# Kernel optimization log

Hardware: AMD Instinct MI355X
Metric: run time of the kernel (lower is better)

## Reference

```python
import jax, jax.numpy as jnp
import numpy as np

B, S, HID = 2, 2048, 2048
NH, NKV, D = 16, 4, 128  # heads, kv heads, dim_per_head
ROPE_BASE = 10000.0


def setup_inputs() -> dict:
    key = jax.random.key(0)
    ks = jax.random.split(key, 5)
    x = jax.random.normal(ks[0], (B, S, HID), jnp.float32)
    wq = jax.random.normal(ks[1], (HID, NH * D), jnp.float32) * 0.02
    wk = jax.random.normal(ks[2], (HID, NKV * D), jnp.float32) * 0.02
    wv = jax.random.normal(ks[3], (HID, NKV * D), jnp.float32) * 0.02
    wo = jax.random.normal(ks[4], (NH * D, HID), jnp.float32) * 0.02
    inv_freq = 1.0 / (ROPE_BASE ** (jnp.arange(0, D, 2, dtype=jnp.float32) / D))
    freqs = jnp.outer(jnp.arange(S, dtype=jnp.float32), inv_freq)  # [S, D/2]
    cos, sin = jnp.cos(freqs), jnp.sin(freqs)
    mask = jnp.tril(jnp.ones((S, S), dtype=bool))  # causal, True = attend
    return {"x": x, "wq": wq, "wk": wk, "wv": wv, "wo": wo,
            "cos": cos, "sin": sin, "mask": mask}


def _rope_interleave(t, cos, sin):
    # t: [B, H, S, D]; cos/sin: [S, D/2]; interleaved pairs (even, odd)
    te, to = t[..., ::2], t[..., 1::2]
    c, s = cos[None, None], sin[None, None]
    re = te * c - to * s
    ro = to * c + te * s
    return jnp.stack([re, ro], axis=-1).reshape(t.shape)


def reference(x, wq, wk, wv, wo, cos, sin, mask):
    b, s, _ = x.shape
    # QKV projections + shape(): [B, S, hid] -> [B, H, S, D]
    q = (x @ wq).reshape(b, s, NH, D).transpose(0, 2, 1, 3)
    k = (x @ wk).reshape(b, s, NKV, D).transpose(0, 2, 1, 3)
    v = (x @ wv).reshape(b, s, NKV, D).transpose(0, 2, 1, 3)
    q = _rope_interleave(q, cos, sin)
    k = _rope_interleave(k, cos, sin)
    # GQA: repeat each kv head heads//heads_kv times consecutively
    rep = NH // NKV
    k = jnp.repeat(k, rep, axis=1)
    v = jnp.repeat(v, rep, axis=1)
    scores = jnp.einsum('bhqd,bhkd->bhqk', q, k) * (D ** -0.5)
    scores = scores.astype(jnp.float32)
    scores = jnp.where(mask[None, None], scores, jnp.finfo(jnp.float32).min)
    attn = jax.nn.softmax(scores, axis=-1).astype(x.dtype)
    ctx = jnp.einsum('bhqk,bhkd->bhqd', attn, v)
    ctx = ctx.transpose(0, 2, 1, 3).reshape(b, s, NH * D)  # unshape()
    return ctx @ wo
```

## Files before the change

kernel.cpp:

```cpp
#include <hip/hip_runtime.h>
#include <hip/hip_bf16.h>
#include <math.h>

#define S_LEN 2048
#define HIDW 2048
#define NHEAD 16
#define NKVH 4
#define HD 128
#define NB 2
#define MROWS (NB * S_LEN)
#define QKVN (NHEAD * HD + 2 * NKVH * HD)
#define KOFF (NHEAD * HD)
#define VOFF (NHEAD * HD + NKVH * HD)

typedef __bf16 bf16_t;
typedef __bf16 bf16x8_t __attribute__((ext_vector_type(8)));
typedef float f32x4_t __attribute__((ext_vector_type(4)));

__device__ __forceinline__ void gload_lds16(const bf16_t* g, bf16_t* l) {
  __builtin_amdgcn_global_load_lds(
      (const __attribute__((address_space(1))) void*)g,
      (__attribute__((address_space(3))) void*)l, 16, 0, 0);
}

__device__ __forceinline__ f32x4_t zero4() {
  f32x4_t z = {0.f, 0.f, 0.f, 0.f};
  return z;
}

__device__ __forceinline__ float fexp2(float x) {
#if __has_builtin(__builtin_amdgcn_exp2f)
  return __builtin_amdgcn_exp2f(x);
#else
  return exp2f(x);
#endif
}

__global__ __launch_bounds__(256) void k_cvt8(const float* __restrict__ in,
                                              bf16_t* __restrict__ out, int n8) {
  int i = blockIdx.x * 256 + threadIdx.x;
  if (i >= n8) return;
  const float4* p = (const float4*)(in + (size_t)i * 8);
  float4 a = p[0], b = p[1];
  bf16x8_t r;
  r[0] = (bf16_t)a.x; r[1] = (bf16_t)a.y; r[2] = (bf16_t)a.z; r[3] = (bf16_t)a.w;
  r[4] = (bf16_t)b.x; r[5] = (bf16_t)b.y; r[6] = (bf16_t)b.z; r[7] = (bf16_t)b.w;
  *(bf16x8_t*)(out + (size_t)i * 8) = r;
}

__global__ __launch_bounds__(256) void k_tr_cvt(const float* __restrict__ in,
                                                bf16_t* __restrict__ out, int R, int C) {
  __shared__ float t[32][33];
  int c0 = blockIdx.x * 32, r0 = blockIdx.y * 32;
  int tx = threadIdx.x & 31, ty = threadIdx.x >> 5;
#pragma unroll
  for (int rr = ty; rr < 32; rr += 8) t[rr][tx] = in[(size_t)(r0 + rr) * C + c0 + tx];
  __syncthreads();
#pragma unroll
  for (int rr = ty; rr < 32; rr += 8)
    out[(size_t)(c0 + rr) * R + r0 + tx] = (bf16_t)t[tx][rr];
}

__global__ __launch_bounds__(512, 2) void k_gemm_qkv8(const bf16_t* __restrict__ A,
                                                      const bf16_t* __restrict__ Bt,
                                                      bf16_t* __restrict__ qkv,
                                                      const float* __restrict__ cosT,
                                                      const float* __restrict__ sinT) {
  __shared__ bf16_t As[2][16384];
  __shared__ bf16_t Bs[2][16384];
  const int K = HIDW, N = QKVN;
  int tid = threadIdx.x;
  int lane = tid & 63, wid = tid >> 6;
  int l15 = lane & 15, lg = lane >> 4;
  int wrb = (wid >> 2) * 128;
  int wcb = (wid & 3) * 64;
  int ah = wid >> 2;
  int bh2 = wcb >> 7;
  int brow0 = wcb & 64;

  int qx = gridDim.x >> 3;
  int lin = blockIdx.x;
  int wg = (lin & 7) * qx + (lin >> 3);
  int row0 = (wg / 12) * 256, col0 = (wg % 12) * 256;

  int srow = tid >> 3;
  int scol = ((tid & 7) ^ (srow & 7)) * 8;
  const bf16_t* Ag = A + (size_t)(row0 + srow) * K + scol;
  const bf16_t* Bg = Bt + (size_t)(col0 + srow) * K + scol;

  f32x4_t acc[8][4];
#pragma unroll
  for (int i = 0; i < 8; i++)
#pragma unroll
    for (int j = 0; j < 4; j++) acc[i][j] = zero4();

  int xr = (l15 & 7) << 4;
  const int nk = K >> 6;

  auto stA = [&](int tt, int h, int u) {
    gload_lds16(Ag + (size_t)(h * 128 + u * 64) * K + (size_t)tt * 64,
                As[tt & 1] + h * 8192 + u * 4096 + tid * 8);
  };
  auto stB = [&](int tt, int h, int u) {
    gload_lds16(Bg + (size_t)(h * 128 + u * 64) * K + (size_t)tt * 64,
                Bs[tt & 1] + h * 8192 + u * 4096 + tid * 8);
  };

  stB(0, 0, 0); stB(0, 0, 1); stA(0, 0, 0); stA(0, 0, 1);
  stB(0, 1, 0); stB(0, 1, 1); stA(0, 1, 0); stA(0, 1, 1);
  stB(1, 0, 0); stB(1, 0, 1); stA(1, 0, 0); stA(1, 0, 1);
  stB(1, 1, 0); stB(1, 1, 1);
  asm volatile("s_waitcnt vmcnt(10)" ::: "memory");
  __builtin_amdgcn_s_barrier();
  __builtin_amdgcn_sched_barrier(0);

  for (int t = 0; t < nk; t++) {
    const char* Ac = (const char*)As[t & 1] + ah * 16384;
    const char* Bc = (const char*)Bs[t & 1] + bh2 * 16384;

    bf16x8_t af0[4][2], bfr[4][2];
#pragma unroll
    for (int i = 0; i < 4; i++) {
      int row = i * 16 + l15;
#pragma unroll
      for (int kk = 0; kk < 2; kk++)
        af0[i][kk] = *(const bf16x8_t*)(Ac + ((row * 128 + kk * 64 + lg * 16) ^ xr));
    }
#pragma unroll
    for (int j = 0; j < 2; j++) {
      int row = brow0 + j * 16 + l15;
#pragma unroll
      for (int kk = 0; kk < 2; kk++)
        bfr[j][kk] = *(const bf16x8_t*)(Bc + ((row * 128 + kk * 64 + lg * 16) ^ xr));
    }
    if (t + 1 < nk) { stA(t + 1, 1, 0); stA(t + 1, 1, 1); }
    __builtin_amdgcn_s_barrier();
    asm volatile("s_waitcnt lgkmcnt(0)" ::: "memory");
    __builtin_amdgcn_sched_barrier(0);
    __builtin_amdgcn_s_setprio(1);
#pragma unroll
    for (int i = 0; i < 4; i++)
#pragma unroll
      for (int j = 0; j < 2; j++)
#pragma unroll
        for (int kk = 0; kk < 2; kk++)
          acc[i][j] = __builtin_amdgcn_mfma_f32_16x16x32_bf16(af0[i][kk], bfr[j][kk],
                                                              acc[i][j], 0, 0, 0);
    __builtin_amdgcn_s_setprio(0);
    __builtin_amdgcn_s_barrier();

#pragma unroll
    for (int j = 2; j < 4; j++) {
      int row = brow0 + j * 16 + l15;
#pragma unroll
      for (int kk = 0; kk < 2; kk++)
        bfr[j][kk] = *(const bf16x8_t*)(Bc + ((row * 128 + kk * 64 + lg * 16) ^ xr));
    }
    __builtin_amdgcn_s_barrier();
    asm volatile("s_waitcnt lgkmcnt(0)" ::: "memory");
    __builtin_amdgcn_sched_barrier(0);
    __builtin_amdgcn_s_setprio(1);
#pragma unroll
    for (int i = 0; i < 4; i++)
#pragma unroll
      for (int j = 2; j < 4; j++)
#pragma unroll
        for (int kk = 0; kk < 2; kk++)
          acc[i][j] = __builtin_amdgcn_mfma_f32_16x16x32_bf16(af0[i][kk], bfr[j][kk],
                                                              acc[i][j], 0, 0, 0);
    __builtin_amdgcn_s_setprio(0);
    __builtin_amdgcn_s_barrier();

    bf16x8_t af1[4][2];
#pragma unroll
    for (int i = 0; i < 4; i++) {
      int row = 64 + i * 16 + l15;
#pragma unroll
      for (int kk = 0; kk < 2; kk++)
        af1[i][kk] = *(const bf16x8_t*)(Ac + ((row * 128 + kk * 64 + lg * 16) ^ xr));
    }
    if (t + 2 < nk) { stB(t + 2, 0, 0); stB(t + 2, 0, 1); }
    __builtin_amdgcn_s_barrier();
    asm volatile("s_waitcnt lgkmcnt(0)" ::: "memory");
    __builtin_amdgcn_sched_barrier(0);
    __builtin_amdgcn_s_setprio(1);
#pragma unroll
    for (int i = 0; i < 4; i++)
#pragma unroll
      for (int j = 0; j < 2; j++)
#pragma unroll
        for (int kk = 0; kk < 2; kk++)
          acc[4 + i][j] = __builtin_amdgcn_mfma_f32_16x16x32_bf16(
              af1[i][kk], bfr[j][kk], acc[4 + i][j], 0, 0, 0);
    __builtin_amdgcn_s_setprio(0);
    __builtin_amdgcn_s_barrier();

    if (t + 2 < nk) { stA(t + 2, 0, 0); stA(t + 2, 0, 1); stB(t + 2, 1, 0); stB(t + 2, 1, 1); }
    __builtin_amdgcn_s_barrier();
    __builtin_amdgcn_s_setprio(1);
#pragma unroll
    for (int i = 0; i < 4; i++)
#pragma unroll
      for (int j = 2; j < 4; j++)
#pragma unroll
        for (int kk = 0; kk < 2; kk++)
          acc[4 + i][j] = __builtin_amdgcn_mfma_f32_16x16x32_bf16(
              af1[i][kk], bfr[j][kk], acc[4 + i][j], 0, 0, 0);
    __builtin_amdgcn_s_setprio(0);
    if (t + 2 < nk) asm volatile("s_waitcnt vmcnt(10)" ::: "memory");
    else            asm volatile("s_waitcnt vmcnt(0)" ::: "memory");
    __builtin_amdgcn_s_barrier();
    __builtin_amdgcn_sched_barrier(0);
  }

  if (col0 < VOFF) {
    int sbase = row0 & (S_LEN - 1);
    bf16_t* cosL = &As[0][0];
    bf16_t* sinL = &Bs[0][0];
#pragma unroll
    for (int k = 0; k < 8; k++) {
      gload_lds16((const bf16_t*)(cosT + (size_t)sbase * 64 + k * 2048 + tid * 4),
                  cosL + k * 4096 + tid * 8);
      gload_lds16((const bf16_t*)(sinT + (size_t)sbase * 64 + k * 2048 + tid * 4),
                  sinL + k * 4096 + tid * 8);
    }
    asm volatile("s_waitcnt vmcnt(0)" ::: "memory");
    __builtin_amdgcn_s_barrier();
    const float* cosF = (const float*)cosL;
    const float* sinF = (const float*)sinL;
    const float QS = 0.08838834764831845f * 1.4426950408889634f;
#pragma unroll
    for (int i = 0; i < 8; i++) {
#pragma unroll
      for (int j = 0; j < 4; j++) {
        int c = col0 + wcb + j * 16 + l15;
        int rlb = wrb + ((i < 4) ? i * 16 : 64 + (i - 4) * 16) + lg * 4;
        float scale = (c < KOFF) ? QS : 1.0f;
        int p0 = (c & 127) >> 1;
        int codd = c & 1;
#pragma unroll
        for (int qd = 0; qd < 4; qd++) {
          int rl = rlb + qd;
          float self = acc[i][j][qd];
          float other = __shfl_xor(self, 1);
          float cv = cosF[rl * 64 + p0], sv = sinF[rl * 64 + p0];
          float outv = codd ? (self * cv + other * sv) : (self * cv - other * sv);
          ((bf16_t*)qkv)[(size_t)(row0 + rl) * N + c] = (bf16_t)(outv * scale);
        }
      }
    }
  } else {
#pragma unroll
    for (int i = 0; i < 8; i++) {
#pragma unroll
      for (int j = 0; j < 4; j++) {
        int r = row0 + wrb + ((i < 4) ? i * 16 : 64 + (i - 4) * 16) + lg * 4;
        int c = col0 + wcb + j * 16 + l15;
#pragma unroll
        for (int qd = 0; qd < 4; qd++)
          qkv[(size_t)(r + qd) * N + c] = (bf16_t)acc[i][j][qd];
      }
    }
  }
}

__global__ __launch_bounds__(512, 2) void k_gemm_out(const bf16_t* __restrict__ A,
                                                     const bf16_t* __restrict__ Bt,
                                                     float* __restrict__ Cout) {
  __shared__ bf16_t As[2][128 * 64];
  __shared__ bf16_t Bs[2][256 * 64];
  const int K = KOFF, N = HIDW;
  int tid = threadIdx.x;
  int lane = tid & 63, wid = tid >> 6;
  int l15 = lane & 15, lg = lane >> 4;
  int wrb = (wid >> 2) * 64;
  int wcb = (wid & 3) * 64;

  int qx = gridDim.x >> 3;
  int lin = blockIdx.x;
  int wg = (lin & 7) * qx + (lin >> 3);
  int row0 = (wg >> 3) * 128, col0 = (wg & 7) * 256;

  int srow = tid >> 3;
  int scol = ((tid & 7) ^ (srow & 7)) * 8;
  const bf16_t* Ag = A + (size_t)(row0 + srow) * K + scol;
  const bf16_t* Bg = Bt + (size_t)(col0 + srow) * K + scol;

  f32x4_t acc[4][4];
#pragma unroll
  for (int i = 0; i < 4; i++)
#pragma unroll
    for (int j = 0; j < 4; j++) acc[i][j] = zero4();

  int xr = (l15 & 7) << 4;
  const int nk = K >> 6;

  auto stA = [&](int tt, int u) {
    gload_lds16(Ag + (size_t)u * 64 * K + (size_t)tt * 64, As[tt & 1] + u * 4096 + tid * 8);
  };
  auto stB = [&](int tt, int u) {
    gload_lds16(Bg + (size_t)u * 64 * K + (size_t)tt * 64, Bs[tt & 1] + u * 4096 + tid * 8);
  };

  for (int tt = 0; tt < 2; tt++) {
    for (int u = 0; u < 2; u++) stA(tt, u);
    for (int u = 0; u < 4; u++) stB(tt, u);
  }
  asm volatile("s_waitcnt vmcnt(6)" ::: "memory");
  __builtin_amdgcn_s_barrier();
  __builtin_amdgcn_sched_barrier(0);

  for (int t = 0; t < nk; t++) {
    const char* Ac = (const char*)As[t & 1];
    const char* Bc = (const char*)Bs[t & 1];
    bool pf = (t + 2 < nk);

    bf16x8_t af0[4][2], bfr[4][2];
#pragma unroll
    for (int i = 0; i < 4; i++) {
      int row = wrb + i * 16 + l15;
#pragma unroll
      for (int kk = 0; kk < 2; kk++)
        af0[i][kk] = *(const bf16x8_t*)(Ac + ((row * 128 + kk * 64 + lg * 16) ^ xr));
    }
#pragma unroll
    for (int j = 0; j < 4; j++) {
      int rowb = wcb + j * 16 + l15;
#pragma unroll
      for (int kk = 0; kk < 2; kk++)
        bfr[j][kk] = *(const bf16x8_t*)(Bc + ((rowb * 128 + kk * 64 + lg * 16) ^ xr));
    }
    __builtin_amdgcn_s_barrier();
    __builtin_amdgcn_s_setprio(1);
#pragma unroll
    for (int i = 0; i < 4; i++)
#pragma unroll
      for (int kk = 0; kk < 2; kk++)
        acc[i][0] = __builtin_amdgcn_mfma_f32_16x16x32_bf16(af0[i][kk], bfr[0][kk],
                                                            acc[i][0], 0, 0, 0);
    __builtin_amdgcn_s_setprio(0);

    if (pf) { stA(t + 2, 0); stA(t + 2, 1); }
    __builtin_amdgcn_s_barrier();
    __builtin_amdgcn_s_setprio(1);
#pragma unroll
    for (int i = 0; i < 4; i++)
#pragma unroll
      for (int kk = 0; kk < 2; kk++)
        acc[i][1] = __builtin_amdgcn_mfma_f32_16x16x32_bf16(af0[i][kk], bfr[1][kk],
                                                            acc[i][1], 0, 0, 0);
    __builtin_amdgcn_s_setprio(0);

    if (pf) { stB(t + 2, 0); stB(t + 2, 1); }
    __builtin_amdgcn_s_barrier();
    __builtin_amdgcn_s_setprio(1);
#pragma unroll
    for (int i = 0; i < 4; i++)
#pragma unroll
      for (int kk = 0; kk < 2; kk++)
        acc[i][2] = __builtin_amdgcn_mfma_f32_16x16x32_bf16(af0[i][kk], bfr[2][kk],
                                                            acc[i][2], 0, 0, 0);
    __builtin_amdgcn_s_setprio(0);

    if (pf) { stB(t + 2, 2); stB(t + 2, 3); }
    __builtin_amdgcn_s_barrier();
    __builtin_amdgcn_s_setprio(1);
#pragma unroll
    for (int i = 0; i < 4; i++)
#pragma unroll
      for (int kk = 0; kk < 2; kk++)
        acc[i][3] = __builtin_amdgcn_mfma_f32_16x16x32_bf16(af0[i][kk], bfr[3][kk],
                                                            acc[i][3], 0, 0, 0);
    __builtin_amdgcn_s_setprio(0);

    if (t + 1 < nk) {
      if (pf) asm volatile("s_waitcnt vmcnt(6)" ::: "memory");
      else    asm volatile("s_waitcnt vmcnt(0)" ::: "memory");
    }
    __builtin_amdgcn_s_barrier();
    __builtin_amdgcn_sched_barrier(0);
  }

#pragma unroll
  for (int i = 0; i < 4; i++) {
#pragma unroll
    for (int j = 0; j < 4; j++) {
      int r = row0 + wrb + i * 16 + lg * 4;
      int c = col0 + wcb + j * 16 + l15;
#pragma unroll
      for (int qd = 0; qd < 4; qd++)
        Cout[(size_t)(r + qd) * N + c] = acc[i][j][qd];
    }
  }
}

__global__ __launch_bounds__(256) void k_vt(const bf16_t* __restrict__ qkv,
                                            bf16_t* __restrict__ vt) {
  __shared__ bf16_t t[32][33];
  int s0 = blockIdx.x * 32;
  int dt = (blockIdx.y & 3) * 32;
  int h = blockIdx.y >> 2;
  int b = blockIdx.z;
  int tx = threadIdx.x & 31, ty = threadIdx.x >> 5;
#pragma unroll
  for (int rr = ty; rr < 32; rr += 8)
    t[rr][tx] = qkv[(size_t)(b * S_LEN + s0 + rr) * QKVN + VOFF + h * HD + dt + tx];
  __syncthreads();
#pragma unroll
  for (int rr = ty; rr < 32; rr += 8)
    vt[((size_t)((b * NKVH + h) * HD + dt + rr)) * S_LEN + s0 + tx] = t[tx][rr];
}

__global__ __launch_bounds__(256, 2) void k_attn(const bf16_t* __restrict__ qkv,
                                                 const bf16_t* __restrict__ vt,
                                                 bf16_t* __restrict__ ctx) {
  __shared__ bf16_t Ks[2 * 64 * 128];
  __shared__ bf16_t Vs[2 * 128 * 64];
  __shared__ bf16_t plds[4][16 * 72];

  int tid = threadIdx.x;
  int lane = tid & 63, wid = tid >> 6;
  int idx = blockIdx.x;
  int bh = idx & 31;
  int qg = 31 - (idx >> 5);
  int b = bh >> 4, h = bh & 15;
  int kvh = h >> 2;
  int q0 = qg * 64 + wid * 16;
  int l15 = lane & 15, lg = lane >> 4;

  const bf16_t* Kbase = qkv + (size_t)(b * S_LEN) * QKVN + KOFF + kvh * HD;
  const bf16_t* Vbase = vt + (size_t)(b * NKVH + kvh) * HD * S_LEN;

  const bf16_t* Qp = qkv + (size_t)(b * S_LEN + q0 + l15) * QKVN + h * HD + lg * 8;
  bf16x8_t aq[4];
#pragma unroll
  for (int kk = 0; kk < 4; kk++) aq[kk] = *(const bf16x8_t*)(Qp + kk * 32);

  int Ls[4], Lk[4], Lv[4];
#pragma unroll
  for (int u = 0; u < 4; u++) {
    int L = u * 4096 + tid * 16;
    Ls[u] = L >> 1;
    Lk[u] = L ^ (((L >> 8) & 7) << 4);
    Lv[u] = L ^ (((L >> 7) & 7) << 4);
  }

  f32x4_t o[8];
#pragma unroll
  for (int j = 0; j < 8; j++) o[j] = zero4();
  float ms = -INFINITY, lsum = 0.f;

  bf16_t* pbuf = &plds[wid][0];
  int xr = (l15 & 7) << 4;
  int ntiles = qg + 1;
  int qcol = q0 + l15;

#pragma unroll
  for (int u = 0; u < 4; u++) {
    gload_lds16(Kbase + (size_t)(Lk[u] >> 8) * QKVN + ((Lk[u] & 255) >> 1), Ks + Ls[u]);
    gload_lds16(Vbase + (size_t)(Lv[u] >> 7) * S_LEN + ((Lv[u] & 127) >> 1), Vs + Ls[u]);
  }
  __syncthreads();

  for (int t = 0; t < ntiles; t++) {
    int kv0 = t * 64;
    if (t + 1 < ntiles) {
      const bf16_t* Kn = Kbase + (size_t)(kv0 + 64) * QKVN;
      const bf16_t* Vn = Vbase + kv0 + 64;
      int bo = ((t + 1) & 1) * 8192;
#pragma unroll
      for (int u = 0; u < 4; u++) {
        gload_lds16(Kn + (size_t)(Lk[u] >> 8) * QKVN + ((Lk[u] & 255) >> 1), Ks + bo + Ls[u]);
        gload_lds16(Vn + (size_t)(Lv[u] >> 7) * S_LEN + ((Lv[u] & 127) >> 1), Vs + bo + Ls[u]);
      }
    }
    const char* Kb = (const char*)Ks + (t & 1) * 16384;
    const char* Vb = (const char*)Vs + (t & 1) * 16384;

    f32x4_t sacc[4];
#pragma unroll
    for (int cg = 0; cg < 4; cg++) sacc[cg] = zero4();
#pragma unroll
    for (int cg = 0; cg < 4; cg++) {
#pragma unroll
      for (int kk = 0; kk < 4; kk++) {
        int boff = ((cg * 16 + l15) * 256 + kk * 64 + lg * 16) ^ xr;
        bf16x8_t bk = *(const bf16x8_t*)(Kb + boff);
        sacc[cg] = __builtin_amdgcn_mfma_f32_16x16x32_bf16(bk, aq[kk], sacc[cg], 0, 0, 0);
      }
    }
    if (kv0 + 63 > q0) {
#pragma unroll
      for (int cg = 0; cg < 4; cg++) {
#pragma unroll
        for (int i = 0; i < 4; i++) {
          int kvg = kv0 + cg * 16 + lg * 4 + i;
          if (kvg > qcol) sacc[cg][i] = -1e30f;
        }
      }
    }
    float pmax = sacc[0][0];
#pragma unroll
    for (int cg = 0; cg < 4; cg++)
#pragma unroll
      for (int i = 0; i < 4; i++) pmax = fmaxf(pmax, sacc[cg][i]);
    pmax = fmaxf(pmax, __shfl_xor(pmax, 16));
    pmax = fmaxf(pmax, __shfl_xor(pmax, 32));
    if (__any(pmax - ms > 8.0f)) {
      float nm = fmaxf(ms, pmax);
      float sc = fexp2(ms - nm);
      ms = nm;
      lsum *= sc;
      float sci[4];
#pragma unroll
      for (int i = 0; i < 4; i++) sci[i] = __shfl(sc, lg * 4 + i);
#pragma unroll
      for (int j = 0; j < 8; j++)
#pragma unroll
        for (int i = 0; i < 4; i++) o[j][i] *= sci[i];
    }
    float ls = 0.f;
#pragma unroll
    for (int cg = 0; cg < 4; cg++)
#pragma unroll
      for (int i = 0; i < 4; i++) {
        sacc[cg][i] = fexp2(sacc[cg][i] - ms);
        ls += sacc[cg][i];
      }
    ls += __shfl_xor(ls, 16);
    ls += __shfl_xor(ls, 32);
    lsum += ls;
#pragma unroll
    for (int cg = 0; cg < 4; cg++)
#pragma unroll
      for (int i = 0; i < 4; i++)
        pbuf[l15 * 72 + cg * 16 + lg * 4 + i] = (bf16_t)sacc[cg][i];
    __builtin_amdgcn_wave_barrier();
    bf16x8_t pa0 = *(const bf16x8_t*)(pbuf + l15 * 72 + lg * 8);
    bf16x8_t pa1 = *(const bf16x8_t*)(pbuf + l15 * 72 + 32 + lg * 8);
    __builtin_amdgcn_wave_barrier();
#pragma unroll
    for (int j = 0; j < 8; j++) {
      int d = j * 16 + l15;
      int bo0 = (d * 128 + lg * 16) ^ xr;
      int bo1 = (d * 128 + 64 + lg * 16) ^ xr;
      o[j] = __builtin_amdgcn_mfma_f32_16x16x32_bf16(
          pa0, *(const bf16x8_t*)(Vb + bo0), o[j], 0, 0, 0);
      o[j] = __builtin_amdgcn_mfma_f32_16x16x32_bf16(
          pa1, *(const bf16x8_t*)(Vb + bo1), o[j], 0, 0, 0);
    }
    __syncthreads();
  }

  bf16_t* Cp = ctx + (size_t)(b * S_LEN + q0) * KOFF + h * HD;
#pragma unroll
  for (int i = 0; i < 4; i++) {
    float inv = 1.f / __shfl(lsum, lg * 4 + i);
    int row = lg * 4 + i;
#pragma unroll
    for (int j = 0; j < 8; j++)
      Cp[(size_t)row * KOFF + j * 16 + l15] = (bf16_t)(o[j][i] * inv);
  }
}

extern "C" void kernel_launch(void* const* d_in, const int* in_sizes, int n_in,
                              void* d_out, int out_size, void* d_ws, size_t ws_size,
                              hipStream_t stream) {
  const float* x = (const float*)d_in[0];
  const float* wq = (const float*)d_in[1];
  const float* wk = (const float*)d_in[2];
  const float* wv = (const float*)d_in[3];
  const float* wo = (const float*)d_in[4];
  const float* cosT = (const float*)d_in[5];
  const float* sinT = (const float*)d_in[6];

  bf16_t* xb = (bf16_t*)d_ws;
  bf16_t* wqkvT = xb + (size_t)MROWS * HIDW;
  bf16_t* woT = wqkvT + (size_t)QKVN * HIDW;
  bf16_t* qkv = woT + (size_t)HIDW * HIDW;
  bf16_t* vtb = qkv + (size_t)MROWS * QKVN;

  k_cvt8<<<MROWS * HIDW / 8 / 256, 256, 0, stream>>>(x, xb, MROWS * HIDW / 8);
  k_tr_cvt<<<dim3(KOFF / 32, HIDW / 32), 256, 0, stream>>>(wq, wqkvT, HIDW, KOFF);
  k_tr_cvt<<<dim3((NKVH * HD) / 32, HIDW / 32), 256, 0, stream>>>(
      wk, wqkvT + (size_t)KOFF * HIDW, HIDW, NKVH * HD);
  k_tr_cvt<<<dim3((NKVH * HD) / 32, HIDW / 32), 256, 0, stream>>>(
      wv, wqkvT + (size_t)VOFF * HIDW, HIDW, NKVH * HD);
  k_tr_cvt<<<dim3(HIDW / 32, KOFF / 32), 256, 0, stream>>>(wo, woT, KOFF, HIDW);
  k_gemm_qkv8<<<(MROWS / 256) * (QKVN / 256), 512, 0, stream>>>(
      xb, wqkvT, qkv, cosT, sinT);
  k_vt<<<dim3(S_LEN / 32, 4 * NKVH, NB), 256, 0, stream>>>(qkv, vtb);
  k_attn<<<32 * 32, 256, 0, stream>>>(qkv, vtb, xb);
  k_gemm_out<<<(MROWS / 128) * (HIDW / 256), 512, 0, stream>>>(xb, woT,
                                                               (float*)d_out);
}
```

Measured before the change: 205.6 us.

## Restructure QKV and output GEMM pipelines, fuse weight transposes, prioritize attention MFMAs

The QKV GEMM drops its split-half LDS scheduling with per-stage lgkmcnt waits and switches to a simpler four-phase loop that prefetches two tiles ahead. The output GEMM tile shrinks from 128x256 to 128x128, which doubles the grid and should improve CU occupancy and load balance. The three Q/K/V weight transpose launches are merged into one kernel. The attention MFMA sections get s_setprio raised. These changes trade fewer launches and more parallelism for possible scheduling differences in the hand-tuned GEMM.

```diff
diff --git a/kernel.cpp b/kernel.cpp
--- a/kernel.cpp
+++ b/kernel.cpp
@@ -61,22 +61,39 @@
     out[(size_t)(c0 + rr) * R + r0 + tx] = (bf16_t)t[tx][rr];
 }
 
-__global__ __launch_bounds__(512, 2) void k_gemm_qkv8(const bf16_t* __restrict__ A,
-                                                      const bf16_t* __restrict__ Bt,
-                                                      bf16_t* __restrict__ qkv,
-                                                      const float* __restrict__ cosT,
-                                                      const float* __restrict__ sinT) {
-  __shared__ bf16_t As[2][16384];
-  __shared__ bf16_t Bs[2][16384];
+__global__ __launch_bounds__(256) void k_tr_qkvw(const float* __restrict__ wq,
+                                                 const float* __restrict__ wk,
+                                                 const float* __restrict__ wv,
+                                                 bf16_t* __restrict__ out) {
+  __shared__ float t[32][33];
+  int c0 = blockIdx.x * 32, r0 = blockIdx.y * 32;
+  const float* src;
+  int C, cb;
+  if (c0 < KOFF)      { src = wq; C = 2048; cb = c0; }
+  else if (c0 < VOFF) { src = wk; C = 512;  cb = c0 - KOFF; }
+  else                { src = wv; C = 512;  cb = c0 - VOFF; }
+  int tx = threadIdx.x & 31, ty = threadIdx.x >> 5;
+#pragma unroll
+  for (int rr = ty; rr < 32; rr += 8) t[rr][tx] = src[(size_t)(r0 + rr) * C + cb + tx];
+  __syncthreads();
+#pragma unroll
+  for (int rr = ty; rr < 32; rr += 8)
+    out[(size_t)(c0 + rr) * HIDW + r0 + tx] = (bf16_t)t[tx][rr];
+}
+
+__global__ __launch_bounds__(512, 2) void k_gemm_qkv(const bf16_t* __restrict__ A,
+                                                     const bf16_t* __restrict__ Bt,
+                                                     bf16_t* __restrict__ qkv,
+                                                     const float* __restrict__ cosT,
+                                                     const float* __restrict__ sinT) {
+  __shared__ bf16_t As[2][256 * 64];
+  __shared__ bf16_t Bs[2][256 * 64];
   const int K = HIDW, N = QKVN;
   int tid = threadIdx.x;
   int lane = tid & 63, wid = tid >> 6;
   int l15 = lane & 15, lg = lane >> 4;
   int wrb = (wid >> 2) * 128;
   int wcb = (wid & 3) * 64;
-  int ah = wid >> 2;
-  int bh2 = wcb >> 7;
-  int brow0 = wcb & 64;
 
   int qx = gridDim.x >> 3;
   int lin = blockIdx.x;
@@ -97,46 +114,42 @@
   int xr = (l15 & 7) << 4;
   const int nk = K >> 6;
 
-  auto stA = [&](int tt, int h, int u) {
-    gload_lds16(Ag + (size_t)(h * 128 + u * 64) * K + (size_t)tt * 64,
-                As[tt & 1] + h * 8192 + u * 4096 + tid * 8);
+  auto stA = [&](int tt, int u) {
+    gload_lds16(Ag + (size_t)u * 64 * K + (size_t)tt * 64, As[tt & 1] + u * 4096 + tid * 8);
   };
-  auto stB = [&](int tt, int h, int u) {
-    gload_lds16(Bg + (size_t)(h * 128 + u * 64) * K + (size_t)tt * 64,
-                Bs[tt & 1] + h * 8192 + u * 4096 + tid * 8);
+  auto stB = [&](int tt, int u) {
+    gload_lds16(Bg + (size_t)u * 64 * K + (size_t)tt * 64, Bs[tt & 1] + u * 4096 + tid * 8);
   };
 
-  stB(0, 0, 0); stB(0, 0, 1); stA(0, 0, 0); stA(0, 0, 1);
-  stB(0, 1, 0); stB(0, 1, 1); stA(0, 1, 0); stA(0, 1, 1);
-  stB(1, 0, 0); stB(1, 0, 1); stA(1, 0, 0); stA(1, 0, 1);
-  stB(1, 1, 0); stB(1, 1, 1);
-  asm volatile("s_waitcnt vmcnt(10)" ::: "memory");
+  for (int tt = 0; tt < 2; tt++) {
+    for (int u = 0; u < 4; u++) stA(tt, u);
+    for (int u = 0; u < 4; u++) stB(tt, u);
+  }
+  asm volatile("s_waitcnt vmcnt(8)" ::: "memory");
   __builtin_amdgcn_s_barrier();
   __builtin_amdgcn_sched_barrier(0);
 
   for (int t = 0; t < nk; t++) {
-    const char* Ac = (const char*)As[t & 1] + ah * 16384;
-    const char* Bc = (const char*)Bs[t & 1] + bh2 * 16384;
+    const char* Ac = (const char*)As[t & 1];
+    const char* Bc = (const char*)Bs[t & 1];
+    bool pf = (t + 2 < nk);
 
     bf16x8_t af0[4][2], bfr[4][2];
 #pragma unroll
     for (int i = 0; i < 4; i++) {
-      int row = i * 16 + l15;
+      int row = wrb + i * 16 + l15;
 #pragma unroll
       for (int kk = 0; kk < 2; kk++)
         af0[i][kk] = *(const bf16x8_t*)(Ac + ((row * 128 + kk * 64 + lg * 16) ^ xr));
     }
 #pragma unroll
-    for (int j = 0; j < 2; j++) {
-      int row = brow0 + j * 16 + l15;
-#pragma unroll
-      for (int kk = 0; kk < 2; kk++)
-        bfr[j][kk] = *(const bf16x8_t*)(Bc + ((row * 128 + kk * 64 + lg * 16) ^ xr));
-    }
-    if (t + 1 < nk) { stA(t + 1, 1, 0); stA(t + 1, 1, 1); }
-    __builtin_amdgcn_s_barrier();
-    asm volatile("s_waitcnt lgkmcnt(0)" ::: "memory");
-    __builtin_amdgcn_sched_barrier(0);
+    for (int jn = 0; jn < 4; jn++) {
+      int rowb = wcb + jn * 16 + l15;
+#pragma unroll
+      for (int kk = 0; kk < 2; kk++)
+        bfr[jn][kk] = *(const bf16x8_t*)(Bc + ((rowb * 128 + kk * 64 + lg * 16) ^ xr));
+    }
+    __builtin_amdgcn_s_barrier();
     __builtin_amdgcn_s_setprio(1);
 #pragma unroll
     for (int i = 0; i < 4; i++)
@@ -147,42 +160,30 @@
           acc[i][j] = __builtin_amdgcn_mfma_f32_16x16x32_bf16(af0[i][kk], bfr[j][kk],
                                                               acc[i][j], 0, 0, 0);
     __builtin_amdgcn_s_setprio(0);
-    __builtin_amdgcn_s_barrier();
-
-#pragma unroll
-    for (int j = 2; j < 4; j++) {
-      int row = brow0 + j * 16 + l15;
-#pragma unroll
-      for (int kk = 0; kk < 2; kk++)
-        bfr[j][kk] = *(const bf16x8_t*)(Bc + ((row * 128 + kk * 64 + lg * 16) ^ xr));
-    }
-    __builtin_amdgcn_s_barrier();
-    asm volatile("s_waitcnt lgkmcnt(0)" ::: "memory");
-    __builtin_amdgcn_sched_barrier(0);
+
+    if (pf) { stA(t + 2, 0); stA(t + 2, 2); }
+    __builtin_amdgcn_s_barrier();
     __builtin_amdgcn_s_setprio(1);
 #pragma unroll
     for (int i = 0; i < 4; i++)
 #pragma unroll
-      for (int j = 2; j < 4; j++)
+      for (int j = 0; j < 2; j++)
 #pragma unroll
         for (int kk = 0; kk < 2; kk++)
-          acc[i][j] = __builtin_amdgcn_mfma_f32_16x16x32_bf16(af0[i][kk], bfr[j][kk],
-                                                              acc[i][j], 0, 0, 0);
-    __builtin_amdgcn_s_setprio(0);
-    __builtin_amdgcn_s_barrier();
+          acc[i][2 + j] = __builtin_amdgcn_mfma_f32_16x16x32_bf16(
+              af0[i][kk], bfr[2 + j][kk], acc[i][2 + j], 0, 0, 0);
+    __builtin_amdgcn_s_setprio(0);
 
     bf16x8_t af1[4][2];
 #pragma unroll
     for (int i = 0; i < 4; i++) {
-      int row = 64 + i * 16 + l15;
+      int row = wrb + 64 + i * 16 + l15;
 #pragma unroll
       for (int kk = 0; kk < 2; kk++)
         af1[i][kk] = *(const bf16x8_t*)(Ac + ((row * 128 + kk * 64 + lg * 16) ^ xr));
     }
-    if (t + 2 < nk) { stB(t + 2, 0, 0); stB(t + 2, 0, 1); }
-    __builtin_amdgcn_s_barrier();
-    asm volatile("s_waitcnt lgkmcnt(0)" ::: "memory");
-    __builtin_amdgcn_sched_barrier(0);
+    if (pf) { stB(t + 2, 0); stB(t + 2, 1); }
+    __builtin_amdgcn_s_barrier();
     __builtin_amdgcn_s_setprio(1);
 #pragma unroll
     for (int i = 0; i < 4; i++)
@@ -193,22 +194,24 @@
           acc[4 + i][j] = __builtin_amdgcn_mfma_f32_16x16x32_bf16(
               af1[i][kk], bfr[j][kk], acc[4 + i][j], 0, 0, 0);
     __builtin_amdgcn_s_setprio(0);
-    __builtin_amdgcn_s_barrier();
-
-    if (t + 2 < nk) { stA(t + 2, 0, 0); stA(t + 2, 0, 1); stB(t + 2, 1, 0); stB(t + 2, 1, 1); }
+
+    if (pf) { stB(t + 2, 2); stB(t + 2, 3); stA(t + 2, 1); stA(t + 2, 3); }
     __builtin_amdgcn_s_barrier();
     __builtin_amdgcn_s_setprio(1);
 #pragma unroll
     for (int i = 0; i < 4; i++)
 #pragma unroll
-      for (int j = 2; j < 4; j++)
+      for (int j = 0; j < 2; j++)
 #pragma unroll
         for (int kk = 0; kk < 2; kk++)
-          acc[4 + i][j] = __builtin_amdgcn_mfma_f32_16x16x32_bf16(
-              af1[i][kk], bfr[j][kk], acc[4 + i][j], 0, 0, 0);
-    __builtin_amdgcn_s_setprio(0);
-    if (t + 2 < nk) asm volatile("s_waitcnt vmcnt(10)" ::: "memory");
-    else            asm volatile("s_waitcnt vmcnt(0)" ::: "memory");
+          acc[4 + i][2 + j] = __builtin_amdgcn_mfma_f32_16x16x32_bf16(
+              af1[i][kk], bfr[2 + j][kk], acc[4 + i][2 + j], 0, 0, 0);
+    __builtin_amdgcn_s_setprio(0);
+
+    if (t + 1 < nk) {
+      if (pf) asm volatile("s_waitcnt vmcnt(8)" ::: "memory");
+      else    asm volatile("s_waitcnt vmcnt(0)" ::: "memory");
+    }
     __builtin_amdgcn_s_barrier();
     __builtin_amdgcn_sched_barrier(0);
   }
@@ -245,7 +248,7 @@
           float other = __shfl_xor(self, 1);
           float cv = cosF[rl * 64 + p0], sv = sinF[rl * 64 + p0];
           float outv = codd ? (self * cv + other * sv) : (self * cv - other * sv);
-          ((bf16_t*)qkv)[(size_t)(row0 + rl) * N + c] = (bf16_t)(outv * scale);
+          qkv[(size_t)(row0 + rl) * N + c] = (bf16_t)(outv * scale);
         }
       }
     }
@@ -268,29 +271,29 @@
                                                      const bf16_t* __restrict__ Bt,
                                                      float* __restrict__ Cout) {
   __shared__ bf16_t As[2][128 * 64];
-  __shared__ bf16_t Bs[2][256 * 64];
+  __shared__ bf16_t Bs[2][128 * 64];
   const int K = KOFF, N = HIDW;
   int tid = threadIdx.x;
   int lane = tid & 63, wid = tid >> 6;
   int l15 = lane & 15, lg = lane >> 4;
   int wrb = (wid >> 2) * 64;
-  int wcb = (wid & 3) * 64;
+  int wcb = (wid & 3) * 32;
 
   int qx = gridDim.x >> 3;
   int lin = blockIdx.x;
   int wg = (lin & 7) * qx + (lin >> 3);
-  int row0 = (wg >> 3) * 128, col0 = (wg & 7) * 256;
+  int row0 = (wg >> 4) * 128, col0 = (wg & 15) * 128;
 
   int srow = tid >> 3;
   int scol = ((tid & 7) ^ (srow & 7)) * 8;
   const bf16_t* Ag = A + (size_t)(row0 + srow) * K + scol;
   const bf16_t* Bg = Bt + (size_t)(col0 + srow) * K + scol;
 
-  f32x4_t acc[4][4];
+  f32x4_t acc[4][2];
 #pragma unroll
   for (int i = 0; i < 4; i++)
 #pragma unroll
-    for (int j = 0; j < 4; j++) acc[i][j] = zero4();
+    for (int j = 0; j < 2; j++) acc[i][j] = zero4();
 
   int xr = (l15 & 7) << 4;
   const int nk = K >> 6;
@@ -303,10 +306,9 @@
   };
 
   for (int tt = 0; tt < 2; tt++) {
-    for (int u = 0; u < 2; u++) stA(tt, u);
-    for (int u = 0; u < 4; u++) stB(tt, u);
-  }
-  asm volatile("s_waitcnt vmcnt(6)" ::: "memory");
+    stA(tt, 0); stA(tt, 1); stB(tt, 0); stB(tt, 1);
+  }
+  asm volatile("s_waitcnt vmcnt(4)" ::: "memory");
   __builtin_amdgcn_s_barrier();
   __builtin_amdgcn_sched_barrier(0);
 
@@ -315,16 +317,16 @@
     const char* Bc = (const char*)Bs[t & 1];
     bool pf = (t + 2 < nk);
 
-    bf16x8_t af0[4][2], bfr[4][2];
+    bf16x8_t af[4][2], bfr[2][2];
 #pragma unroll
     for (int i = 0; i < 4; i++) {
       int row = wrb + i * 16 + l15;
 #pragma unroll
       for (int kk = 0; kk < 2; kk++)
-        af0[i][kk] = *(const bf16x8_t*)(Ac + ((row * 128 + kk * 64 + lg * 16) ^ xr));
-    }
-#pragma unroll
-    for (int j = 0; j < 4; j++) {
+        af[i][kk] = *(const bf16x8_t*)(Ac + ((row * 128 + kk * 64 + lg * 16) ^ xr));
+    }
+#pragma unroll
+    for (int j = 0; j < 2; j++) {
       int rowb = wcb + j * 16 + l15;
 #pragma unroll
       for (int kk = 0; kk < 2; kk++)
@@ -336,45 +338,23 @@
     for (int i = 0; i < 4; i++)
 #pragma unroll
       for (int kk = 0; kk < 2; kk++)
-        acc[i][0] = __builtin_amdgcn_mfma_f32_16x16x32_bf16(af0[i][kk], bfr[0][kk],
+        acc[i][0] = __builtin_amdgcn_mfma_f32_16x16x32_bf16(af[i][kk], bfr[0][kk],
                                                             acc[i][0], 0, 0, 0);
     __builtin_amdgcn_s_setprio(0);
 
-    if (pf) { stA(t + 2, 0); stA(t + 2, 1); }
+    if (pf) { stA(t + 2, 0); stA(t + 2, 1); stB(t + 2, 0); stB(t + 2, 1); }
     __builtin_amdgcn_s_barrier();
     __builtin_amdgcn_s_setprio(1);
 #pragma unroll
     for (int i = 0; i < 4; i++)
 #pragma unroll
       for (int kk = 0; kk < 2; kk++)
-        acc[i][1] = __builtin_amdgcn_mfma_f32_16x16x32_bf16(af0[i][kk], bfr[1][kk],
+        acc[i][1] = __builtin_amdgcn_mfma_f32_16x16x32_bf16(af[i][kk], bfr[1][kk],
                                                             acc[i][1], 0, 0, 0);
     __builtin_amdgcn_s_setprio(0);
 
-    if (pf) { stB(t + 2, 0); stB(t + 2, 1); }
-    __builtin_amdgcn_s_barrier();
-    __builtin_amdgcn_s_setprio(1);
-#pragma unroll
-    for (int i = 0; i < 4; i++)
-#pragma unroll
-      for (int kk = 0; kk < 2; kk++)
-        acc[i][2] = __builtin_amdgcn_mfma_f32_16x16x32_bf16(af0[i][kk], bfr[2][kk],
-                                                            acc[i][2], 0, 0, 0);
-    __builtin_amdgcn_s_setprio(0);
-
-    if (pf) { stB(t + 2, 2); stB(t + 2, 3); }
-    __builtin_amdgcn_s_barrier();
-    __builtin_amdgcn_s_setprio(1);
-#pragma unroll
-    for (int i = 0; i < 4; i++)
-#pragma unroll
-      for (int kk = 0; kk < 2; kk++)
-        acc[i][3] = __builtin_amdgcn_mfma_f32_16x16x32_bf16(af0[i][kk], bfr[3][kk],
-                                                            acc[i][3], 0, 0, 0);
-    __builtin_amdgcn_s_setprio(0);
-
     if (t + 1 < nk) {
-      if (pf) asm volatile("s_waitcnt vmcnt(6)" ::: "memory");
+      if (pf) asm volatile("s_waitcnt vmcnt(4)" ::: "memory");
       else    asm volatile("s_waitcnt vmcnt(0)" ::: "memory");
     }
     __builtin_amdgcn_s_barrier();
@@ -384,7 +364,7 @@
 #pragma unroll
   for (int i = 0; i < 4; i++) {
 #pragma unroll
-    for (int j = 0; j < 4; j++) {
+    for (int j = 0; j < 2; j++) {
       int r = row0 + wrb + i * 16 + lg * 4;
       int c = col0 + wcb + j * 16 + l15;
 #pragma unroll
@@ -480,6 +460,7 @@
     f32x4_t sacc[4];
 #pragma unroll
     for (int cg = 0; cg < 4; cg++) sacc[cg] = zero4();
+    __builtin_amdgcn_s_setprio(1);
 #pragma unroll
     for (int cg = 0; cg < 4; cg++) {
 #pragma unroll
@@ -489,6 +470,7 @@
         sacc[cg] = __builtin_amdgcn_mfma_f32_16x16x32_bf16(bk, aq[kk], sacc[cg], 0, 0, 0);
       }
     }
+    __builtin_amdgcn_s_setprio(0);
     if (kv0 + 63 > q0) {
 #pragma unroll
       for (int cg = 0; cg < 4; cg++) {
@@ -539,6 +521,7 @@
     bf16x8_t pa0 = *(const bf16x8_t*)(pbuf + l15 * 72 + lg * 8);
     bf16x8_t pa1 = *(const bf16x8_t*)(pbuf + l15 * 72 + 32 + lg * 8);
     __builtin_amdgcn_wave_barrier();
+    __builtin_amdgcn_s_setprio(1);
 #pragma unroll
     for (int j = 0; j < 8; j++) {
       int d = j * 16 + l15;
@@ -549,6 +532,7 @@
       o[j] = __builtin_amdgcn_mfma_f32_16x16x32_bf16(
           pa1, *(const bf16x8_t*)(Vb + bo1), o[j], 0, 0, 0);
     }
+    __builtin_amdgcn_s_setprio(0);
     __syncthreads();
   }
 
@@ -581,16 +565,12 @@
   bf16_t* vtb = qkv + (size_t)MROWS * QKVN;
 
   k_cvt8<<<MROWS * HIDW / 8 / 256, 256, 0, stream>>>(x, xb, MROWS * HIDW / 8);
-  k_tr_cvt<<<dim3(KOFF / 32, HIDW / 32), 256, 0, stream>>>(wq, wqkvT, HIDW, KOFF);
-  k_tr_cvt<<<dim3((NKVH * HD) / 32, HIDW / 32), 256, 0, stream>>>(
-      wk, wqkvT + (size_t)KOFF * HIDW, HIDW, NKVH * HD);
-  k_tr_cvt<<<dim3((NKVH * HD) / 32, HIDW / 32), 256, 0, stream>>>(
-      wv, wqkvT + (size_t)VOFF * HIDW, HIDW, NKVH * HD);
+  k_tr_qkvw<<<dim3(QKVN / 32, HIDW / 32), 256, 0, stream>>>(wq, wk, wv, wqkvT);
   k_tr_cvt<<<dim3(HIDW / 32, KOFF / 32), 256, 0, stream>>>(wo, woT, KOFF, HIDW);
-  k_gemm_qkv8<<<(MROWS / 256) * (QKVN / 256), 512, 0, stream>>>(
+  k_gemm_qkv<<<(MROWS / 256) * (QKVN / 256), 512, 0, stream>>>(
       xb, wqkvT, qkv, cosT, sinT);
   k_vt<<<dim3(S_LEN / 32, 4 * NKVH, NB), 256, 0, stream>>>(qkv, vtb);
   k_attn<<<32 * 32, 256, 0, stream>>>(qkv, vtb, xb);
-  k_gemm_out<<<(MROWS / 128) * (HIDW / 256), 512, 0, stream>>>(xb, woT,
+  k_gemm_out<<<(MROWS / 128) * (HIDW / 128), 512, 0, stream>>>(xb, woT,
                                                                (float*)d_out);
 }
```

Measured after the change: 194.5 us. -5.4%, faster.
